# Kernel tuning notes

Hardware: AMD Instinct MI355X
Metric: run time of the kernel (lower is better)

## Reference

```python
import jax, jax.numpy as jnp
import numpy as np

DECAY = 0.99


def setup_inputs() -> dict:
    key = jax.random.key(0)
    k1, k2, k3 = jax.random.split(key, 3)
    B, L, D, N = 8, 2048, 512, 1024
    x = jax.random.normal(k1, (B, L, D), dtype=jnp.float32)
    codebook = jax.random.normal(k2, (N, D), dtype=jnp.float32)
    ema_weight = jax.random.normal(k3, (N, D), dtype=jnp.float32)
    counts = jnp.ones((N,), dtype=jnp.float32)
    return {"x": x, "codebook": codebook, "ema_weight": ema_weight, "counts": counts}


def reference(x, codebook, ema_weight, counts):
    # x: [B, L, D]; codebook/ema_weight: [N, D]; counts: [N]
    n_tokens = codebook.shape[0]
    # avoids materializing the [B,L,N,D] difference tensor of the naive form)
    x_sq = jnp.sum(x * x, axis=-1, keepdims=True)            # [B, L, 1]
    c_sq = jnp.sum(codebook * codebook, axis=-1)             # [N]
    xc = jnp.einsum('bld,nd->bln', x, codebook)              # [B, L, N]
    distances = jnp.sqrt(jnp.maximum(x_sq - 2.0 * xc + c_sq, 0.0))
    indices = jnp.argmin(distances, axis=-1)                 # [B, L]
    encodings = jax.nn.one_hot(indices, n_tokens, dtype=jnp.float32)  # [B, L, N]
    # train=True branch: EMA codebook update
    counts_new = DECAY * counts + (1.0 - DECAY) * jnp.sum(encodings, axis=(0, 1))
    dw = jnp.einsum('bln,bld->nd', encodings, x)             # [N, D]
    ema_new = DECAY * ema_weight + (1.0 - DECAY) * dw
    codebook_new = ema_new / counts_new[:, None]
    # quantization with straight-through estimator
    quantized = jnp.einsum('bln,nd->bld', encodings, codebook_new)  # [B, L, D]
    quantized = x + jax.lax.stop_gradient(quantized - x)
    # optax.l2_loss(x, quantized) = 0.5 * (x - quantized)^2
    codebook_loss = jnp.mean(0.5 * jnp.square(x - quantized))
    return quantized, codebook_loss, indices
```

## Files before the change

### kernel.cpp

```cpp
#include <hip/hip_runtime.h>
#include <hip/hip_bf16.h>

constexpr int Dd   = 512;
constexpr int Nn   = 1024;
constexpr int Ttok = 16384;
constexpr float DECAYc = 0.99f;
constexpr float GAP = 3.0f;
constexpr int CH = 16;

typedef short bf16x8 __attribute__((ext_vector_type(8)));
typedef float f32x4  __attribute__((ext_vector_type(4)));

__device__ inline unsigned cvtpk(float lo, float hi) {
  unsigned r;
  asm("v_cvt_pk_bf16_f32 %0, %1, %2" : "=v"(r) : "v"(lo), "v"(hi));
  return r;
}

constexpr int NB_CB = 256, NB_Z = 32, NB_X = 2048;
constexpr int ZF4 = 131329;
__global__ __launch_bounds__(256) void k_prep(
    const float* __restrict__ cb, const float* __restrict__ x,
    unsigned short* __restrict__ cbh, float* __restrict__ csq,
    unsigned short* __restrict__ xh, float4* __restrict__ zbase) {
  const int b = blockIdx.x, tid = threadIdx.x;
  if (b < NB_CB) {
    const int n = b * 4 + (tid >> 6), l = tid & 63;
    const float4* r = (const float4*)(cb + (size_t)n * Dd);
    float4 a = r[l], c = r[l + 64];
    float ss = a.x*a.x + a.y*a.y + a.z*a.z + a.w*a.w
             + c.x*c.x + c.y*c.y + c.z*c.z + c.w*c.w;
    uint2 ua, uc;
    ua.x = cvtpk(a.x, a.y); ua.y = cvtpk(a.z, a.w);
    uc.x = cvtpk(c.x, c.y); uc.y = cvtpk(c.z, c.w);
    ((uint2*)(cbh + (size_t)n * Dd))[l]      = ua;
    ((uint2*)(cbh + (size_t)n * Dd))[l + 64] = uc;
#pragma unroll
    for (int o = 32; o; o >>= 1) ss += __shfl_down(ss, o);
    if (l == 0) csq[n] = ss;
  } else if (b < NB_CB + NB_Z) {
    const float4 z = make_float4(0.f, 0.f, 0.f, 0.f);
    for (int i = (b - NB_CB) * 256 + tid; i < ZF4; i += NB_Z * 256)
      zbase[i] = z;
  } else {
    const int bx = b - (NB_CB + NB_Z);
#pragma unroll
    for (int k = 0; k < 2; ++k) {
      const int i = bx * 512 + k * 256 + tid;
      float4 a = ((const float4*)x)[i * 2];
      float4 c = ((const float4*)x)[i * 2 + 1];
      uint4 o;
      o.x = cvtpk(a.x, a.y); o.y = cvtpk(a.z, a.w);
      o.z = cvtpk(c.x, c.y); o.w = cvtpk(c.z, c.w);
      ((uint4*)xh)[i] = o;
    }
  }
}

__global__ __launch_bounds__(256) void k_gemm_scores(
    const unsigned short* __restrict__ cbh, const unsigned short* __restrict__ xh,
    const float* __restrict__ csq, float4* __restrict__ part) {
  __shared__ unsigned short As[2][128 * 64];
  __shared__ unsigned short Bs[2][128 * 64];
  const int tid = threadIdx.x;
  const int w = tid >> 6, l = tid & 63;
  const int b = blockIdx.x;
  const int s = (b & 7) * 128 + (b >> 3);
  const int cm = s & 7;
  const int tn = s >> 3;
  const int wr = w >> 1, wc = w & 1;

  const int srow = tid >> 3;
  const int xorw = (tid >> 3) & 7;
  const int scol = ((tid & 7) ^ xorw) * 8;

  f32x4 acc[4][4] = {};

  const unsigned short* gA0 = cbh + (size_t)(cm * 128) * Dd;
  const unsigned short* gB0 = xh  + (size_t)(tn * 128) * Dd;

#define ISSUE(KC, BUF) do {                                                   \
    const int k0_ = (KC) * 64;                                                \
    _Pragma("unroll")                                                         \
    for (int c = 0; c < 4; ++c) {                                             \
      const unsigned short* ga = gA0 + (size_t)(c * 32 + srow) * Dd + k0_ + scol; \
      const unsigned short* gb = gB0 + (size_t)(c * 32 + srow) * Dd + k0_ + scol; \
      char* la = (char*)&As[BUF][0] + c * 4096 + w * 1024;                    \
      char* lb = (char*)&Bs[BUF][0] + c * 4096 + w * 1024;                    \
      __builtin_amdgcn_global_load_lds((const __attribute__((address_space(1))) void*)ga, \
                                       (__attribute__((address_space(3))) void*)la, 16, 0, 0); \
      __builtin_amdgcn_global_load_lds((const __attribute__((address_space(1))) void*)gb, \
                                       (__attribute__((address_space(3))) void*)lb, 16, 0, 0); \
    }                                                                         \
  } while (0)

  ISSUE(0, 0);

  for (int kc = 0; kc < Dd / 64; ++kc) {
    __syncthreads();
    if (kc + 1 < Dd / 64) ISSUE(kc + 1, (kc + 1) & 1);
    const unsigned short* Ab = &As[kc & 1][0];
    const unsigned short* Bb = &Bs[kc & 1][0];
#pragma unroll
    for (int ks = 0; ks < 2; ++ks) {
      const int ra = l & 15;
      const int rx = l & 7;
      const int kbs = ((ks * 4 + (l >> 4)) ^ rx) * 8;
      bf16x8 af[4], bfr[4];
#pragma unroll
      for (int m = 0; m < 4; ++m)
        af[m] = *(const bf16x8*)&Ab[(wr * 64 + m * 16 + ra) * 64 + kbs];
#pragma unroll
      for (int n = 0; n < 4; ++n)
        bfr[n] = *(const bf16x8*)&Bb[(wc * 64 + n * 16 + ra) * 64 + kbs];
#pragma unroll
      for (int m = 0; m < 4; ++m)
#pragma unroll
        for (int n = 0; n < 4; ++n)
          acc[m][n] = __builtin_amdgcn_mfma_f32_16x16x32_bf16(af[m], bfr[n], acc[m][n], 0, 0, 0);
    }
  }
#undef ISSUE

  const int base4 = wr * 64 + (l >> 4) * 4;
  float4 cs[4];
#pragma unroll
  for (int m = 0; m < 4; ++m)
    cs[m] = *(const float4*)&csq[cm * 128 + base4 + m * 16];

  const int slot = cm * 2 + wr;
  const int tok0 = tn * 128 + wc * 64 + (l & 15);

#pragma unroll
  for (int n = 0; n < 4; ++n) {
    float v0 = 3.4e38f, v1 = 3.4e38f, v2 = 3.4e38f;
    int i0 = 0x7fffffff, i1 = 0x7fffffff;
#pragma unroll
    for (int m = 0; m < 4; ++m) {
#pragma unroll
      for (int r = 0; r < 4; ++r) {
        float sv = fmaf(-2.0f, acc[m][n][r], ((const float*)&cs[m])[r]);
        int idx = cm * 128 + base4 + m * 16 + r;
        if (sv < v0)      { v2 = v1; v1 = v0; i1 = i0; v0 = sv; i0 = idx; }
        else if (sv < v1) { v2 = v1; v1 = sv; i1 = idx; }
        else if (sv < v2) { v2 = sv; }
      }
    }
#pragma unroll
    for (int o = 16; o <= 32; o <<= 1) {
      float w0 = __shfl_xor(v0, o), w1 = __shfl_xor(v1, o), w2 = __shfl_xor(v2, o);
      int  j0 = __shfl_xor(i0, o), j1 = __shfl_xor(i1, o);
      bool f = (w0 < v0) || (w0 == v0 && j0 < i0);
      float A0 = f ? w0 : v0, A1 = f ? w1 : v1, A2 = f ? w2 : v2;
      int  Ai0 = f ? j0 : i0, Ai1 = f ? j1 : i1;
      float B0 = f ? v0 : w0, B1 = f ? v1 : w1;
      int  Bi0 = f ? i0 : j0;
      bool g = (A1 < B0) || (A1 == B0 && Ai1 < Bi0);
      v0 = A0; i0 = Ai0;
      v1 = g ? A1 : B0; i1 = g ? Ai1 : Bi0;
      v2 = g ? fminf(A2, B0) : fminf(A1, B1);
    }
    if ((l >> 4) == 0)
      part[(size_t)slot * Ttok + tok0 + n * 16] = make_float4(
          v0, v1, __uint_as_float((unsigned)i0 | ((unsigned)i1 << 16)), v2);
  }
}

__device__ inline void rescore(int n, const float4& xa, const float4& xb,
                               const float* __restrict__ cb,
                               const float* __restrict__ csq, int l,
                               float& bestv, int& besti) {
  const float4* cr = (const float4*)(cb + (size_t)n * Dd);
  float4 ca = cr[l * 2], cc = cr[l * 2 + 1];
  float p = xa.x*ca.x + xa.y*ca.y + xa.z*ca.z + xa.w*ca.w
          + xb.x*cc.x + xb.y*cc.y + xb.z*cc.z + xb.w*cc.w;
#pragma unroll
  for (int o = 32; o; o >>= 1) p += __shfl_xor(p, o);
  float sc = csq[n] - 2.0f * p;
  if (sc < bestv || (sc == bestv && n < besti)) { bestv = sc; besti = n; }
}

__device__ inline void rescore_half(int h, const float* __restrict__ xrow,
                                    const float* __restrict__ cb,
                                    const float* __restrict__ csq, int l,
                                    float& bestv, int& besti) {
  int n = h * 64 + l;
  const float4* cr = (const float4*)(cb + (size_t)n * Dd);
  const float4* xr = (const float4*)xrow;
  float p = 0.f;
#pragma unroll 8
  for (int j = 0; j < 128; ++j) {
    float4 c4 = cr[j], x4 = xr[j];
    p += c4.x*x4.x + c4.y*x4.y + c4.z*x4.z + c4.w*x4.w;
  }
  float sc = csq[n] - 2.0f * p;
#pragma unroll
  for (int o = 1; o < 64; o <<= 1) {
    float ov = __shfl_xor(sc, o); int oi = __shfl_xor(n, o);
    if (ov < sc || (ov == sc && oi < n)) { sc = ov; n = oi; }
  }
  if (sc < bestv || (sc == bestv && n < besti)) { bestv = sc; besti = n; }
}

__global__ __launch_bounds__(256) void k_select(
    const float4* __restrict__ part, const float* __restrict__ x,
    const float* __restrict__ cb, const float* __restrict__ csq,
    int* __restrict__ idxb, float* __restrict__ idxf, float* __restrict__ hist) {
  const int tid = threadIdx.x, wid = tid >> 6, l = tid & 63;
  const int t = blockIdx.x * 4 + wid;
  float v0 = 3.4e38f, v1 = 3.4e38f, v2 = 3.4e38f;
  int i0 = 0x7fffffff, i1 = 0x7fffffff;
  if (l < 16) {
    float4 e = part[(size_t)l * Ttok + t];
    v0 = e.x; v1 = e.y; v2 = e.w;
    unsigned ii = __float_as_uint(e.z);
    i0 = (int)(ii & 0xffff); i1 = (int)(ii >> 16);
  }
  float A0 = v0, A1 = v1; int Ai0 = i0, Ai1 = i1;
#pragma unroll
  for (int o = 1; o < 16; o <<= 1) {
    float w0 = __shfl_xor(A0, o), w1 = __shfl_xor(A1, o);
    int  j0 = __shfl_xor(Ai0, o), j1 = __shfl_xor(Ai1, o);
    bool f = (w0 < A0) || (w0 == A0 && j0 < Ai0);
    float B0 = f ? A0 : w0; int Bi0 = f ? Ai0 : j0;
    float W1 = f ? w1 : A1; int Wi1 = f ? j1 : Ai1;
    if (f) { A0 = w0; Ai0 = j0; }
    bool g = (B0 < W1) || (B0 == W1 && Bi0 < Wi1);
    A1 = g ? B0 : W1; Ai1 = g ? Bi0 : Wi1;
  }
  const float m  = __shfl(A0, 0);
  const float g1 = __shfl(A1, 0);
  const int   gi = __shfl(Ai0, 0);
  int besti;
  if (g1 - m > GAP) {
    besti = gi;
  } else {
    const float thr = m + GAP;
    const float* xrow = x + (size_t)t * Dd;
    const float4* xr = (const float4*)xrow;
    float4 xa = xr[l * 2], xb = xr[l * 2 + 1];
    float bestv = 3.4e38f; besti = 0x7fffffff;
    for (int h = 0; h < 16; ++h) {
      float b0 = __shfl(v0, h);
      if (b0 > thr) continue;
      float b1 = __shfl(v1, h), b2 = __shfl(v2, h);
      int bi0 = __shfl(i0, h), bi1 = __shfl(i1, h);
      if (b2 <= thr) {
        rescore_half(h, xrow, cb, csq, l, bestv, besti);
      } else {
        rescore(bi0, xa, xb, cb, csq, l, bestv, besti);
        if (b1 <= thr) rescore(bi1, xa, xb, cb, csq, l, bestv, besti);
      }
    }
  }
  if (l == 0) {
    idxb[t] = besti;
    idxf[t] = (float)besti;
    atomicAdd(&hist[besti], 1.0f);
  }
}

__global__ __launch_bounds__(256) void k_offsets(const float* __restrict__ hist,
                                                 int* __restrict__ offs,
                                                 int* __restrict__ cursor) {
  __shared__ int wsum[4];
  const int tid = threadIdx.x, l = tid & 63, wd = tid >> 6;
  const int base = tid * 4;
  int c0 = (int)hist[base], c1 = (int)hist[base + 1],
      c2 = (int)hist[base + 2], c3 = (int)hist[base + 3];
  int sum = c0 + c1 + c2 + c3;
  int sc = sum;
#pragma unroll
  for (int o = 1; o < 64; o <<= 1) { int v = __shfl_up(sc, o); if (l >= o) sc += v; }
  if (l == 63) wsum[wd] = sc;
  __syncthreads();
  int wbase = 0;
  for (int i = 0; i < wd; ++i) wbase += wsum[i];
  int e = wbase + sc - sum;
  offs[base] = e;     cursor[base] = e;
  offs[base+1] = e + c0; cursor[base+1] = e + c0;
  offs[base+2] = e + c0 + c1; cursor[base+2] = e + c0 + c1;
  offs[base+3] = e + c0 + c1 + c2; cursor[base+3] = e + c0 + c1 + c2;
}

__global__ __launch_bounds__(256) void k_scatter(const int* __restrict__ idxb,
                                                 int* __restrict__ cursor,
                                                 int* __restrict__ bucket,
                                                 int* __restrict__ bcode) {
  int t = blockIdx.x * 256 + threadIdx.x;
  if (t < Ttok) {
    int n = idxb[t];
    int p = atomicAdd(&cursor[n], 1);
    bucket[p] = t;
    bcode[p] = n;
  }
}

__global__ __launch_bounds__(512) void k_dw_part(
    const float* __restrict__ x, const int* __restrict__ bucket,
    const int* __restrict__ bcode, float* __restrict__ dw) {
  __shared__ int sh_t[CH], sh_n[CH];
  const int tid = threadIdx.x;
  const int p0 = blockIdx.x * CH;
  if (tid < CH) { sh_t[tid] = bucket[p0 + tid]; sh_n[tid] = bcode[p0 + tid]; }
  __syncthreads();
  float v[CH];
#pragma unroll
  for (int j = 0; j < CH; ++j)
    v[j] = x[(size_t)sh_t[j] * Dd + tid];
  float acc = v[0]; int cur = sh_n[0];
#pragma unroll
  for (int j = 1; j < CH; ++j) {
    int n = sh_n[j];
    if (n != cur) { atomicAdd(&dw[(size_t)cur * Dd + tid], acc); acc = 0.f; cur = n; }
    acc += v[j];
  }
  atomicAdd(&dw[(size_t)cur * Dd + tid], acc);
}

__global__ __launch_bounds__(256) void finalize_cb(
    const float* __restrict__ ema, const float* __restrict__ dw,
    const float* __restrict__ counts, const float* __restrict__ hist,
    float* __restrict__ cbnew) {
  int e4 = blockIdx.x * 256 + threadIdx.x;
  int n = e4 >> 7;
  float cnt = DECAYc * counts[n] + (1.0f - DECAYc) * hist[n];
  float inv = 1.0f / cnt;
  float4 e = ((const float4*)ema)[e4];
  float4 d = ((const float4*)dw)[e4];
  float4 o;
  o.x = (DECAYc * e.x + (1.0f - DECAYc) * d.x) * inv;
  o.y = (DECAYc * e.y + (1.0f - DECAYc) * d.y) * inv;
  o.z = (DECAYc * e.z + (1.0f - DECAYc) * d.z) * inv;
  o.w = (DECAYc * e.w + (1.0f - DECAYc) * d.w) * inv;
  ((float4*)cbnew)[e4] = o;
}

__global__ __launch_bounds__(256) void quant_loss(
    const float* __restrict__ x, const float* __restrict__ cbnew,
    const int* __restrict__ idx, float* __restrict__ out_q,
    float* __restrict__ loss) {
  const int e0 = blockIdx.x * 256 + threadIdx.x;
  const int gsz = 524288;
  int n[4]; f32x4 q[4], xv[4];
#pragma unroll
  for (int j = 0; j < 4; ++j) n[j] = idx[(e0 + j * gsz) >> 7];
#pragma unroll
  for (int j = 0; j < 4; ++j) {
    const int e = e0 + j * gsz;
    q[j]  = ((const f32x4*)(cbnew + (size_t)n[j] * Dd))[e & 127];
    xv[j] = ((const f32x4*)x)[e];
  }
  float part = 0.f;
#pragma unroll
  for (int j = 0; j < 4; ++j) {
    __builtin_nontemporal_store(q[j], &((f32x4*)out_q)[e0 + j * gsz]);
    f32x4 d = xv[j] - q[j];
    part += d[0]*d[0] + d[1]*d[1] + d[2]*d[2] + d[3]*d[3];
  }
  __shared__ float red[4];
#pragma unroll
  for (int o = 32; o; o >>= 1) part += __shfl_down(part, o);
  int wid = threadIdx.x >> 6, lane = threadIdx.x & 63;
  if (lane == 0) red[wid] = part;
  __syncthreads();
  if (threadIdx.x == 0) atomicAdd(loss, red[0] + red[1] + red[2] + red[3]);
}

__global__ void loss_final(const float* __restrict__ loss,
                           float* __restrict__ out_loss) {
  *out_loss = loss[0] * (0.5f / (float)((size_t)Ttok * Dd));
}

extern "C" void kernel_launch(void* const* d_in, const int* in_sizes, int n_in,
                              void* d_out, int out_size, void* d_ws, size_t ws_size,
                              hipStream_t stream) {
  const float* x      = (const float*)d_in[0];
  const float* cb     = (const float*)d_in[1];
  const float* ema    = (const float*)d_in[2];
  const float* counts = (const float*)d_in[3];

  float* out      = (float*)d_out;
  float* q_out    = out;
  float* loss_out = out + (size_t)Ttok * Dd;
  float* idxf_out = loss_out + 1;
  float4* part = (float4*)q_out;
  unsigned short* xh = (unsigned short*)(q_out + 2097152);

  float* ws = (float*)d_ws;
  unsigned short* cbh = (unsigned short*)ws;
  float* dw      = ws + 262144;
  float* hist    = ws + 786432;
  float* loss    = ws + 787456;
  float* csq     = ws + 787460;
  int*   offs    = (int*)(ws + 788484);
  int*   cursor  = (int*)(ws + 789508);
  int*   bucket  = (int*)(ws + 790532);
  int*   bcode   = (int*)(ws + 806916);
  int*   idxb    = (int*)(ws + 823300);
  float* cbnew   = ws + 839684;

  k_prep<<<NB_CB + NB_Z + NB_X, 256, 0, stream>>>(cb, x, cbh, csq, xh, (float4*)dw);
  k_gemm_scores<<<(Nn / 128) * (Ttok / 128), 256, 0, stream>>>(cbh, xh, csq, part);
  k_select<<<Ttok / 4, 256, 0, stream>>>(part, x, cb, csq, idxb, idxf_out, hist);
  k_offsets<<<1, 256, 0, stream>>>(hist, offs, cursor);
  k_scatter<<<Ttok / 256, 256, 0, stream>>>(idxb, cursor, bucket, bcode);
  k_dw_part<<<Ttok / CH, 512, 0, stream>>>(x, bucket, bcode, dw);
  finalize_cb<<<(Nn * Dd / 4) / 256, 256, 0, stream>>>(ema, dw, counts, hist, cbnew);
  quant_loss<<<2048, 256, 0, stream>>>(x, cbnew, idxb, q_out, loss);
  loss_final<<<1, 1, 0, stream>>>(loss, loss_out);
}
```

Before: 124.5 us.

## Stage GEMM B tile through registers and fuse codebook finalize into quantize

The score GEMM now loads the token (B) tile through registers and writes it to a single-buffered, unswizzled-source LDS tile, while the codebook (A) tile keeps its direct global-to-LDS double buffering. A second __syncthreads is added per k-step. Separately, the finalize_cb kernel is removed and the EMA/count normalisation is computed inline in quant_loss from ema, dw, counts and hist. This saves one launch and one pass over the codebook, but quant_loss now gathers two rows per element instead of one.

New measurement: 142.4 us. +14.3%, slower.

```diff
diff --git a/kernel.cpp b/kernel.cpp
--- a/kernel.cpp
+++ b/kernel.cpp
@@ -61,7 +61,7 @@
     const unsigned short* __restrict__ cbh, const unsigned short* __restrict__ xh,
     const float* __restrict__ csq, float4* __restrict__ part) {
   __shared__ unsigned short As[2][128 * 64];
-  __shared__ unsigned short Bs[2][128 * 64];
+  __shared__ unsigned short Bs[128 * 64];
   const int tid = threadIdx.x;
   const int w = tid >> 6, l = tid & 63;
   const int b = blockIdx.x;
@@ -72,35 +72,47 @@
 
   const int srow = tid >> 3;
   const int xorw = (tid >> 3) & 7;
-  const int scol = ((tid & 7) ^ xorw) * 8;
+  const int scolA = ((tid & 7) ^ xorw) * 8;
+  const int scolB = (tid & 7) * 8;
+  const int wcolB = scolA;
 
   f32x4 acc[4][4] = {};
 
   const unsigned short* gA0 = cbh + (size_t)(cm * 128) * Dd;
   const unsigned short* gB0 = xh  + (size_t)(tn * 128) * Dd;
 
-#define ISSUE(KC, BUF) do {                                                   \
+  uint4 bq[4];
+#define REGB(KC) do {                                                         \
+    const int k0_ = (KC) * 64;                                                \
+    _Pragma("unroll")                                                         \
+    for (int p = 0; p < 4; ++p)                                               \
+      bq[p] = *(const uint4*)(gB0 + (size_t)(p * 32 + srow) * Dd + k0_ + scolB); \
+  } while (0)
+#define ISSUEA(KC, BUF) do {                                                  \
     const int k0_ = (KC) * 64;                                                \
     _Pragma("unroll")                                                         \
     for (int c = 0; c < 4; ++c) {                                             \
-      const unsigned short* ga = gA0 + (size_t)(c * 32 + srow) * Dd + k0_ + scol; \
-      const unsigned short* gb = gB0 + (size_t)(c * 32 + srow) * Dd + k0_ + scol; \
+      const unsigned short* ga = gA0 + (size_t)(c * 32 + srow) * Dd + k0_ + scolA; \
       char* la = (char*)&As[BUF][0] + c * 4096 + w * 1024;                    \
-      char* lb = (char*)&Bs[BUF][0] + c * 4096 + w * 1024;                    \
       __builtin_amdgcn_global_load_lds((const __attribute__((address_space(1))) void*)ga, \
                                        (__attribute__((address_space(3))) void*)la, 16, 0, 0); \
-      __builtin_amdgcn_global_load_lds((const __attribute__((address_space(1))) void*)gb, \
-                                       (__attribute__((address_space(3))) void*)lb, 16, 0, 0); \
     }                                                                         \
   } while (0)
 
-  ISSUE(0, 0);
+  ISSUEA(0, 0);
+  REGB(0);
 
   for (int kc = 0; kc < Dd / 64; ++kc) {
     __syncthreads();
-    if (kc + 1 < Dd / 64) ISSUE(kc + 1, (kc + 1) & 1);
+#pragma unroll
+    for (int p = 0; p < 4; ++p)
+      *(uint4*)&Bs[(p * 32 + srow) * 64 + wcolB] = bq[p];
+    __syncthreads();
+    if (kc + 1 < Dd / 64) {
+      ISSUEA(kc + 1, (kc + 1) & 1);
+      REGB(kc + 1);
+    }
     const unsigned short* Ab = &As[kc & 1][0];
-    const unsigned short* Bb = &Bs[kc & 1][0];
 #pragma unroll
     for (int ks = 0; ks < 2; ++ks) {
       const int ra = l & 15;
@@ -112,7 +124,7 @@
         af[m] = *(const bf16x8*)&Ab[(wr * 64 + m * 16 + ra) * 64 + kbs];
 #pragma unroll
       for (int n = 0; n < 4; ++n)
-        bfr[n] = *(const bf16x8*)&Bb[(wc * 64 + n * 16 + ra) * 64 + kbs];
+        bfr[n] = *(const bf16x8*)&Bs[(wc * 64 + n * 16 + ra) * 64 + kbs];
 #pragma unroll
       for (int m = 0; m < 4; ++m)
 #pragma unroll
@@ -120,7 +132,8 @@
           acc[m][n] = __builtin_amdgcn_mfma_f32_16x16x32_bf16(af[m], bfr[n], acc[m][n], 0, 0, 0);
     }
   }
-#undef ISSUE
+#undef REGB
+#undef ISSUEA
 
   const int base4 = wr * 64 + (l >> 4) * 4;
   float4 cs[4];
@@ -318,44 +331,34 @@
   atomicAdd(&dw[(size_t)cur * Dd + tid], acc);
 }
 
-__global__ __launch_bounds__(256) void finalize_cb(
-    const float* __restrict__ ema, const float* __restrict__ dw,
-    const float* __restrict__ counts, const float* __restrict__ hist,
-    float* __restrict__ cbnew) {
-  int e4 = blockIdx.x * 256 + threadIdx.x;
-  int n = e4 >> 7;
-  float cnt = DECAYc * counts[n] + (1.0f - DECAYc) * hist[n];
-  float inv = 1.0f / cnt;
-  float4 e = ((const float4*)ema)[e4];
-  float4 d = ((const float4*)dw)[e4];
-  float4 o;
-  o.x = (DECAYc * e.x + (1.0f - DECAYc) * d.x) * inv;
-  o.y = (DECAYc * e.y + (1.0f - DECAYc) * d.y) * inv;
-  o.z = (DECAYc * e.z + (1.0f - DECAYc) * d.z) * inv;
-  o.w = (DECAYc * e.w + (1.0f - DECAYc) * d.w) * inv;
-  ((float4*)cbnew)[e4] = o;
-}
-
 __global__ __launch_bounds__(256) void quant_loss(
-    const float* __restrict__ x, const float* __restrict__ cbnew,
-    const int* __restrict__ idx, float* __restrict__ out_q,
-    float* __restrict__ loss) {
+    const float* __restrict__ x, const float* __restrict__ ema,
+    const float* __restrict__ dw, const float* __restrict__ counts,
+    const float* __restrict__ hist, const int* __restrict__ idx,
+    float* __restrict__ out_q, float* __restrict__ loss) {
   const int e0 = blockIdx.x * 256 + threadIdx.x;
   const int gsz = 524288;
-  int n[4]; f32x4 q[4], xv[4];
+  int n[4];
 #pragma unroll
   for (int j = 0; j < 4; ++j) n[j] = idx[(e0 + j * gsz) >> 7];
+  float inv[4];
+#pragma unroll
+  for (int j = 0; j < 4; ++j)
+    inv[j] = 1.0f / (DECAYc * counts[n[j]] + (1.0f - DECAYc) * hist[n[j]]);
+  f32x4 e4[4], d4[4], xv[4];
 #pragma unroll
   for (int j = 0; j < 4; ++j) {
     const int e = e0 + j * gsz;
-    q[j]  = ((const f32x4*)(cbnew + (size_t)n[j] * Dd))[e & 127];
+    e4[j] = ((const f32x4*)(ema + (size_t)n[j] * Dd))[e & 127];
+    d4[j] = ((const f32x4*)(dw  + (size_t)n[j] * Dd))[e & 127];
     xv[j] = ((const f32x4*)x)[e];
   }
   float part = 0.f;
 #pragma unroll
   for (int j = 0; j < 4; ++j) {
-    __builtin_nontemporal_store(q[j], &((f32x4*)out_q)[e0 + j * gsz]);
-    f32x4 d = xv[j] - q[j];
+    f32x4 q = (DECAYc * e4[j] + (1.0f - DECAYc) * d4[j]) * inv[j];
+    __builtin_nontemporal_store(q, &((f32x4*)out_q)[e0 + j * gsz]);
+    f32x4 d = xv[j] - q;
     part += d[0]*d[0] + d[1]*d[1] + d[2]*d[2] + d[3]*d[3];
   }
   __shared__ float red[4];
@@ -398,7 +401,6 @@
   int*   bucket  = (int*)(ws + 790532);
   int*   bcode   = (int*)(ws + 806916);
   int*   idxb    = (int*)(ws + 823300);
-  float* cbnew   = ws + 839684;
 
   k_prep<<<NB_CB + NB_Z + NB_X, 256, 0, stream>>>(cb, x, cbh, csq, xh, (float4*)dw);
   k_gemm_scores<<<(Nn / 128) * (Ttok / 128), 256, 0, stream>>>(cbh, xh, csq, part);
@@ -406,7 +408,6 @@
   k_offsets<<<1, 256, 0, stream>>>(hist, offs, cursor);
   k_scatter<<<Ttok / 256, 256, 0, stream>>>(idxb, cursor, bucket, bcode);
   k_dw_part<<<Ttok / CH, 512, 0, stream>>>(x, bucket, bcode, dw);
-  finalize_cb<<<(Nn * Dd / 4) / 256, 256, 0, stream>>>(ema, dw, counts, hist, cbnew);
-  quant_loss<<<2048, 256, 0, stream>>>(x, cbnew, idxb, q_out, loss);
+  quant_loss<<<2048, 256, 0, stream>>>(x, ema, dw, counts, hist, idxb, q_out, loss);
   loss_final<<<1, 1, 0, stream>>>(loss, loss_out);
 }
```
